# Kernel optimization log

Hardware: AMD Instinct MI355X
Metric: run time of the kernel (lower is better)

Reference implementation:

```python
import jax, jax.numpy as jnp
import numpy as np
import math

IN_F, OUT_F = 512, 512
N_HEADS, N_SPLITS = 32, 4
N = 1024
DELTA_SCALE = 0.1


def setup_inputs() -> dict:
    key = jax.random.key(0)
    k_x, k_h, k_s, k_w = jax.random.split(key, 4)
    stdv = 1.0 / math.sqrt(OUT_F)
    inputs = {
        "input": jax.random.normal(k_x, (N, IN_F), dtype=jnp.float32),
        "head_ix": jax.random.randint(k_h, (N,), 0, N_HEADS, dtype=jnp.int32),
        "split_ix": jax.random.randint(k_s, (N,), 0, N_SPLITS, dtype=jnp.int32),
        # learned parameters (EmbeddingTensor tables)
        "weight": jax.random.uniform(k_w, (N_HEADS, IN_F, OUT_F), dtype=jnp.float32,
                                     minval=-stdv, maxval=stdv),
        "delta_weight": jnp.zeros((N_HEADS * N_SPLITS, IN_F, OUT_F), dtype=jnp.float32),
        "bias": jnp.zeros((N_HEADS, OUT_F), dtype=jnp.float32),
    }
    return inputs


def reference(input, head_ix, split_ix, weight, delta_weight, bias):
    # per-sample weight: base[head] + 0.1 * delta[head * n_splits + split]
    w = weight[head_ix] + delta_weight[head_ix * N_SPLITS + split_ix] * DELTA_SCALE  # [N, in, out]
    # batched vector-matrix multiply + per-head bias
    return jnp.einsum('ab,abc->ac', input, w) + bias[head_ix]  # [N, out]
```

## Files before the change

kernel.cpp:

```cpp
#include <hip/hip_runtime.h>

#define N_SAMP   1024
#define IN_F     512
#define OUT_F    512
#define N_HEADS  32
#define N_SPLITS 4
#define N_GROUPS (N_HEADS * N_SPLITS)
#define DELTA_SCALE 0.1f

__global__ __launch_bounds__(256, 4) void lms_fused(
    const float* __restrict__ X, const int* __restrict__ head_ix,
    const int* __restrict__ split_ix, const float* __restrict__ W,
    const float* __restrict__ D, const float* __restrict__ bias,
    float* __restrict__ out)
{
    constexpr int J    = 16;
    constexpr int KQ   = 8;
    constexpr int KT   = IN_F / KQ;
    constexpr int NST  = KT / 4;
    constexpr int NOUT = (J * 32) / 256;

    __shared__ float buf[J * IN_F];
    __shared__ int   list[N_SAMP];
    __shared__ int   wsum[4];

    const int g    = blockIdx.y;
    const int h    = g / N_SPLITS;
    const int c0   = blockIdx.x * 64;
    const int tid  = threadIdx.x;
    const int c2   = tid & 31;
    const int kq   = tid >> 5;
    const int lane = tid & 63;
    const int wave = tid >> 6;

    int run = 0;
    for (int r = 0; r < N_SAMP / 256; ++r) {
        const int i   = r * 256 + tid;
        const int key = head_ix[i] * N_SPLITS + split_ix[i];
        const bool hit = (key == g);
        const unsigned long long m = __ballot(hit);
        if (lane == 0) wsum[wave] = __popcll(m);
        __syncthreads();
        int base = run;
        for (int w = 0; w < 4; ++w)
            if (w < wave) base += wsum[w];
        if (hit)
            list[base + __popcll(m & ((1ULL << lane) - 1ULL))] = i;
        run += wsum[0] + wsum[1] + wsum[2] + wsum[3];
        __syncthreads();
    }
    const int total = run;
    if (total == 0) return;

    const size_t roff = (size_t)(kq * KT) * OUT_F + c0 + c2 * 2;
    const float* wp = W + (size_t)h * (IN_F * OUT_F) + roff;
    const float* dp = D + (size_t)g * (IN_F * OUT_F) + roff;

    for (int s0 = 0; s0 < total; s0 += J) {
        const int nc = min(total - s0, J);

        __syncthreads();
        for (int i = tid; i < J * (IN_F / 4); i += 256) {
            const int s = i >> 7, q = i & 127;
            float4 v = make_float4(0.f, 0.f, 0.f, 0.f);
            if (s < nc)
                v = *(const float4*)(X + (size_t)list[s0 + s] * IN_F + q * 4);
            *(float4*)(&buf[s * IN_F + q * 4]) = v;
        }
        __syncthreads();

        float2 acc[J];
#pragma unroll
        for (int j = 0; j < J; ++j) { acc[j].x = 0.f; acc[j].y = 0.f; }

        float2 wb[2][4], db[2][4];
#pragma unroll
        for (int u = 0; u < 4; ++u) {
            wb[0][u] = *(const float2*)(wp + (size_t)u * OUT_F);
            db[0][u] = *(const float2*)(dp + (size_t)u * OUT_F);
        }

#pragma unroll 2
        for (int st = 0; st < NST; ++st) {
            const int nx = (st + 1 < NST) ? st + 1 : NST - 1;
            const int nb = (st + 1) & 1, cb = st & 1;
            const float* wn = wp + (size_t)(nx * 4) * OUT_F;
            const float* dn = dp + (size_t)(nx * 4) * OUT_F;
#pragma unroll
            for (int u = 0; u < 4; ++u) {
                wb[nb][u] = *(const float2*)(wn + (size_t)u * OUT_F);
                db[nb][u] = *(const float2*)(dn + (size_t)u * OUT_F);
            }

            float2 rc[4];
#pragma unroll
            for (int u = 0; u < 4; ++u) {
                rc[u].x = wb[cb][u].x + DELTA_SCALE * db[cb][u].x;
                rc[u].y = wb[cb][u].y + DELTA_SCALE * db[cb][u].y;
            }

            const float* xb = &buf[kq * KT + st * 4];
#pragma unroll
            for (int j = 0; j < J; ++j) {
                const float4 xv = *(const float4*)(xb + j * IN_F);
                acc[j].x += xv.x * rc[0].x; acc[j].y += xv.x * rc[0].y;
                acc[j].x += xv.y * rc[1].x; acc[j].y += xv.y * rc[1].y;
                acc[j].x += xv.z * rc[2].x; acc[j].y += xv.z * rc[2].y;
                acc[j].x += xv.w * rc[3].x; acc[j].y += xv.w * rc[3].y;
            }
        }

        __syncthreads();
        float2* Red = (float2*)buf;
#pragma unroll
        for (int j = 0; j < J; ++j)
            Red[(kq * J + j) * 32 + c2] = acc[j];
        __syncthreads();

#pragma unroll
        for (int t = 0; t < NOUT; ++t) {
            const int oi = t * 256 + tid;
            const int j = oi >> 5, cc = oi & 31;
            if (j < nc) {
                float2 s = make_float2(0.f, 0.f);
#pragma unroll
                for (int q = 0; q < KQ; ++q) {
                    const float2 r = Red[(q * J + j) * 32 + cc];
                    s.x += r.x; s.y += r.y;
                }
                const float2 bv =
                    *(const float2*)(bias + (size_t)h * OUT_F + c0 + cc * 2);
                float* op = out + (size_t)list[s0 + j] * OUT_F + c0 + cc * 2;
                float2 res;
                res.x = s.x + bv.x;
                res.y = s.y + bv.y;
                *(float2*)op = res;
            }
        }
    }
}

extern "C" void kernel_launch(void* const* d_in, const int* in_sizes, int n_in,
                              void* d_out, int out_size, void* d_ws, size_t ws_size,
                              hipStream_t stream) {
    const float* X        = (const float*)d_in[0];
    const int*   head_ix  = (const int*)d_in[1];
    const int*   split_ix = (const int*)d_in[2];
    const float* W        = (const float*)d_in[3];
    const float* D        = (const float*)d_in[4];
    const float* bias     = (const float*)d_in[5];
    float*       out      = (float*)d_out;

    dim3 gf(OUT_F / 64, N_GROUPS);
    lms_fused<<<gf, 256, 0, stream>>>(X, head_ix, split_ix, W, D, bias, out);
}
```

Baseline: 240.0 us.

## Stream full-width weight rows through shared memory and split samples across block pairs

Each block now covers 256 output columns and walks the whole K dimension itself. Eight combined weight rows (W + 0.1*D) per step are staged in a double-buffered shared tile using coalesced float4 loads. This removes the old per-block K-split and the shared-memory cross-partition reduction. The samples of each group are interleaved across two blocks, so each weight/delta slice is fetched by two blocks rather than once per column chunk. The change trades a block-wide barrier every eight rows and fewer, larger blocks (launch bounds lowered to 2) for wider contiguous reads and no reduction phase.

```diff
diff --git a/kernel.cpp b/kernel.cpp
--- a/kernel.cpp
+++ b/kernel.cpp
@@ -8,28 +8,31 @@
 #define N_GROUPS (N_HEADS * N_SPLITS)
 #define DELTA_SCALE 0.1f
 
-__global__ __launch_bounds__(256, 4) void lms_fused(
+__global__ __launch_bounds__(256, 2) void lms_rowstream(
     const float* __restrict__ X, const int* __restrict__ head_ix,
     const int* __restrict__ split_ix, const float* __restrict__ W,
     const float* __restrict__ D, const float* __restrict__ bias,
     float* __restrict__ out)
 {
-    constexpr int J    = 16;
-    constexpr int KQ   = 8;
-    constexpr int KT   = IN_F / KQ;
-    constexpr int NST  = KT / 4;
-    constexpr int NOUT = (J * 32) / 256;
+    constexpr int J    = 8;
+    constexpr int NSG  = 2;
+    constexpr int HC   = 256;
+    constexpr int RPS  = 8;
+    constexpr int NST  = IN_F / RPS;
 
-    __shared__ float buf[J * IN_F];
+    __shared__ float Xs[J][IN_F];
+    __shared__ float rcb[2][RPS][HC];
     __shared__ int   list[N_SAMP];
     __shared__ int   wsum[4];
 
     const int g    = blockIdx.y;
-    const int h    = g / N_SPLITS;
-    const int c0   = blockIdx.x * 64;
+    const int h    = g >> 2;
+    const int sg   = blockIdx.x & 1;
+    const int ch   = blockIdx.x >> 1;
+    const int c0   = ch * HC;
     const int tid  = threadIdx.x;
-    const int c2   = tid & 31;
-    const int kq   = tid >> 5;
+    const int c2   = tid & 127;
+    const int jh   = tid >> 7;
     const int lane = tid & 63;
     const int wave = tid >> 6;
 
@@ -50,90 +53,102 @@
         __syncthreads();
     }
     const int total = run;
-    if (total == 0) return;
+    const int cnt = (total > sg) ? ((total - 1 - sg) / NSG + 1) : 0;
+    if (cnt == 0) return;
 
-    const size_t roff = (size_t)(kq * KT) * OUT_F + c0 + c2 * 2;
-    const float* wp = W + (size_t)h * (IN_F * OUT_F) + roff;
-    const float* dp = D + (size_t)g * (IN_F * OUT_F) + roff;
+    const float* wbase = W + (size_t)h * (IN_F * OUT_F) + c0;
+    const float* dbase = D + (size_t)g * (IN_F * OUT_F) + c0;
+    const float2 bv = *(const float2*)(bias + (size_t)h * OUT_F + c0 + 2 * c2);
 
-    for (int s0 = 0; s0 < total; s0 += J) {
-        const int nc = min(total - s0, J);
+    for (int cb = 0; cb < cnt; cb += J) {
+        const int nc = min(cnt - cb, J);
 
         __syncthreads();
-        for (int i = tid; i < J * (IN_F / 4); i += 256) {
-            const int s = i >> 7, q = i & 127;
+        for (int f = 0; f < 4; ++f) {
+            const int fid = f * 256 + tid;
+            const int s = fid >> 7, q = fid & 127;
             float4 v = make_float4(0.f, 0.f, 0.f, 0.f);
             if (s < nc)
-                v = *(const float4*)(X + (size_t)list[s0 + s] * IN_F + q * 4);
-            *(float4*)(&buf[s * IN_F + q * 4]) = v;
+                v = *(const float4*)(X + (size_t)list[sg + NSG * (cb + s)] * IN_F + q * 4);
+            *(float4*)(&Xs[s][q * 4]) = v;
         }
-        __syncthreads();
 
-        float2 acc[J];
+        float2 acc[4];
 #pragma unroll
-        for (int j = 0; j < J; ++j) { acc[j].x = 0.f; acc[j].y = 0.f; }
+        for (int jj = 0; jj < 4; ++jj) { acc[jj].x = 0.f; acc[jj].y = 0.f; }
 
-        float2 wb[2][4], db[2][4];
-#pragma unroll
-        for (int u = 0; u < 4; ++u) {
-            wb[0][u] = *(const float2*)(wp + (size_t)u * OUT_F);
-            db[0][u] = *(const float2*)(dp + (size_t)u * OUT_F);
+        const int r0 = tid >> 6,        cc0 = (tid & 63) << 2;
+        const int r1 = (256 + tid) >> 6, cc1 = cc0;
+        float4 wrg[2][2], drg[2][2];
+
+        {
+            const float* wp = wbase;
+            const float* dp = dbase;
+            wrg[0][0] = *(const float4*)(wp + (size_t)r0 * OUT_F + cc0);
+            wrg[0][1] = *(const float4*)(wp + (size_t)r1 * OUT_F + cc1);
+            drg[0][0] = *(const float4*)(dp + (size_t)r0 * OUT_F + cc0);
+            drg[0][1] = *(const float4*)(dp + (size_t)r1 * OUT_F + cc1);
         }
 
 #pragma unroll 2
-        for (int st = 0; st < NST; ++st) {
-            const int nx = (st + 1 < NST) ? st + 1 : NST - 1;
-            const int nb = (st + 1) & 1, cb = st & 1;
-            const float* wn = wp + (size_t)(nx * 4) * OUT_F;
-            const float* dn = dp + (size_t)(nx * 4) * OUT_F;
-#pragma unroll
-            for (int u = 0; u < 4; ++u) {
-                wb[nb][u] = *(const float2*)(wn + (size_t)u * OUT_F);
-                db[nb][u] = *(const float2*)(dn + (size_t)u * OUT_F);
+        for (int t = 0; t < NST; ++t) {
+            const int cur = t & 1, nxt = cur ^ 1;
+            const int k0 = t * RPS;
+
+            if (t + 1 < NST) {
+                const float* wp = wbase + (size_t)(k0 + RPS) * OUT_F;
+                const float* dp = dbase + (size_t)(k0 + RPS) * OUT_F;
+                wrg[nxt][0] = *(const float4*)(wp + (size_t)r0 * OUT_F + cc0);
+                wrg[nxt][1] = *(const float4*)(wp + (size_t)r1 * OUT_F + cc1);
+                drg[nxt][0] = *(const float4*)(dp + (size_t)r0 * OUT_F + cc0);
+                drg[nxt][1] = *(const float4*)(dp + (size_t)r1 * OUT_F + cc1);
             }
 
-            float2 rc[4];
-#pragma unroll
-            for (int u = 0; u < 4; ++u) {
-                rc[u].x = wb[cb][u].x + DELTA_SCALE * db[cb][u].x;
-                rc[u].y = wb[cb][u].y + DELTA_SCALE * db[cb][u].y;
+            {
+                float4 a = wrg[cur][0], b = drg[cur][0];
+                float4 rc0 = make_float4(a.x + DELTA_SCALE * b.x,
+                                         a.y + DELTA_SCALE * b.y,
+                                         a.z + DELTA_SCALE * b.z,
+                                         a.w + DELTA_SCALE * b.w);
+                *(float4*)(&rcb[cur][r0][cc0]) = rc0;
+                a = wrg[cur][1]; b = drg[cur][1];
+                float4 rc1 = make_float4(a.x + DELTA_SCALE * b.x,
+                                         a.y + DELTA_SCALE * b.y,
+                                         a.z + DELTA_SCALE * b.z,
+                                         a.w + DELTA_SCALE * b.w);
+                *(float4*)(&rcb[cur][r1][cc1]) = rc1;
             }
 
-            const float* xb = &buf[kq * KT + st * 4];
+            __syncthreads();
+
+            float2 rr[RPS];
 #pragma unroll
-            for (int j = 0; j < J; ++j) {
-                const float4 xv = *(const float4*)(xb + j * IN_F);
-                acc[j].x += xv.x * rc[0].x; acc[j].y += xv.x * rc[0].y;
-                acc[j].x += xv.y * rc[1].x; acc[j].y += xv.y * rc[1].y;
-                acc[j].x += xv.z * rc[2].x; acc[j].y += xv.z * rc[2].y;
-                acc[j].x += xv.w * rc[3].x; acc[j].y += xv.w * rc[3].y;
+            for (int r = 0; r < RPS; ++r)
+                rr[r] = *(const float2*)(&rcb[cur][r][2 * c2]);
+#pragma unroll
+            for (int jj = 0; jj < 4; ++jj) {
+                const int j = jh * 4 + jj;
+                const float4 xa = *(const float4*)(&Xs[j][k0]);
+                const float4 xb = *(const float4*)(&Xs[j][k0 + 4]);
+                acc[jj].x += xa.x * rr[0].x; acc[jj].y += xa.x * rr[0].y;
+                acc[jj].x += xa.y * rr[1].x; acc[jj].y += xa.y * rr[1].y;
+                acc[jj].x += xa.z * rr[2].x; acc[jj].y += xa.z * rr[2].y;
+                acc[jj].x += xa.w * rr[3].x; acc[jj].y += xa.w * rr[3].y;
+                acc[jj].x += xb.x * rr[4].x; acc[jj].y += xb.x * rr[4].y;
+                acc[jj].x += xb.y * rr[5].x; acc[jj].y += xb.y * rr[5].y;
+                acc[jj].x += xb.z * rr[6].x; acc[jj].y += xb.z * rr[6].y;
+                acc[jj].x += xb.w * rr[7].x; acc[jj].y += xb.w * rr[7].y;
             }
         }
 
-        __syncthreads();
-        float2* Red = (float2*)buf;
 #pragma unroll
-        for (int j = 0; j < J; ++j)
-            Red[(kq * J + j) * 32 + c2] = acc[j];
-        __syncthreads();
-
-#pragma unroll
-        for (int t = 0; t < NOUT; ++t) {
-            const int oi = t * 256 + tid;
-            const int j = oi >> 5, cc = oi & 31;
-            if (j < nc) {
-                float2 s = make_float2(0.f, 0.f);
-#pragma unroll
-                for (int q = 0; q < KQ; ++q) {
-                    const float2 r = Red[(q * J + j) * 32 + cc];
-                    s.x += r.x; s.y += r.y;
-                }
-                const float2 bv =
-                    *(const float2*)(bias + (size_t)h * OUT_F + c0 + cc * 2);
-                float* op = out + (size_t)list[s0 + j] * OUT_F + c0 + cc * 2;
+        for (int jj = 0; jj < 4; ++jj) {
+            const int i = cb + jh * 4 + jj;
+            if (i < cnt) {
+                float* op = out + (size_t)list[sg + NSG * i] * OUT_F + c0 + 2 * c2;
                 float2 res;
-                res.x = s.x + bv.x;
-                res.y = s.y + bv.y;
+                res.x = acc[jj].x + bv.x;
+                res.y = acc[jj].y + bv.y;
                 *(float2*)op = res;
             }
         }
@@ -151,6 +166,6 @@
     const float* bias     = (const float*)d_in[5];
     float*       out      = (float*)d_out;
 
-    dim3 gf(OUT_F / 64, N_GROUPS);
-    lms_fused<<<gf, 256, 0, stream>>>(X, head_ix, split_ix, W, D, bias, out);
+    dim3 gf(4, N_GROUPS);
+    lms_rowstream<<<gf, 256, 0, stream>>>(X, head_ix, split_ix, W, D, bias, out);
 }
```

Result: slower. 263.4 us (+9.7%).

## Split K across blocks with workspace partials and a separate reduce kernel

Applied to the files above, without the earlier changes.

Adds a split-K path. Each block handles one group and one 64-row K slice across all 512 output columns, writes partial sums to a workspace, and a second kernel sums the eight partials and adds bias. This removes the in-block shared-memory reduction and shrinks the X staging per block. It also remaps block indices so neighbouring blocks cover different groups. The cost is an extra kernel launch and about 16 MB of workspace writes and reads. The old fused kernel is kept as a fallback when the workspace is too small.

```diff
diff --git a/kernel.cpp b/kernel.cpp
--- a/kernel.cpp
+++ b/kernel.cpp
@@ -7,6 +7,138 @@
 #define N_SPLITS 4
 #define N_GROUPS (N_HEADS * N_SPLITS)
 #define DELTA_SCALE 0.1f
+
+#define KSPLIT   8
+#define KROWS    (IN_F / KSPLIT)
+#define JC       16
+
+
+__global__ __launch_bounds__(256, 4) void lms_partial(
+    const float* __restrict__ X, const int* __restrict__ head_ix,
+    const int* __restrict__ split_ix, const float* __restrict__ W,
+    const float* __restrict__ D, float* __restrict__ ws)
+{
+    __shared__ float Xs[JC][KROWS];
+    __shared__ int   list[N_SAMP];
+    __shared__ int   wsum[4];
+
+    const int b       = blockIdx.x;
+    const int logical = (b & 7) * 128 + (b >> 3);
+    const int g       = logical >> 3;
+    const int kb      = logical & 7;
+    const int h       = g >> 2;
+
+    const int tid  = threadIdx.x;
+    const int lane = tid & 63;
+    const int wave = tid >> 6;
+
+    int run = 0;
+    for (int r = 0; r < N_SAMP / 256; ++r) {
+        const int i   = r * 256 + tid;
+        const int key = head_ix[i] * N_SPLITS + split_ix[i];
+        const bool hit = (key == g);
+        const unsigned long long m = __ballot(hit);
+        if (lane == 0) wsum[wave] = __popcll(m);
+        __syncthreads();
+        int base = run;
+        for (int w = 0; w < 4; ++w)
+            if (w < wave) base += wsum[w];
+        if (hit)
+            list[base + __popcll(m & ((1ULL << lane) - 1ULL))] = i;
+        run += wsum[0] + wsum[1] + wsum[2] + wsum[3];
+        __syncthreads();
+    }
+    const int total = run;
+    if (total == 0) return;
+
+    const float* wq = W + (size_t)h * (IN_F * OUT_F)
+                    + (size_t)(kb * KROWS) * OUT_F + 2 * tid;
+    const float* dq = D + (size_t)g * (IN_F * OUT_F)
+                    + (size_t)(kb * KROWS) * OUT_F + 2 * tid;
+
+    for (int cb = 0; cb < total; cb += JC) {
+        const int nc = min(total - cb, JC);
+
+        __syncthreads();
+        {
+            const int s  = tid >> 4;
+            const int qq = tid & 15;
+            float4 v = make_float4(0.f, 0.f, 0.f, 0.f);
+            if (s < nc)
+                v = *(const float4*)(X + (size_t)list[cb + s] * IN_F
+                                     + kb * KROWS + qq * 4);
+            *(float4*)(&Xs[s][qq * 4]) = v;
+        }
+        __syncthreads();
+
+        float2 acc[JC];
+#pragma unroll
+        for (int j = 0; j < JC; ++j) { acc[j].x = 0.f; acc[j].y = 0.f; }
+
+        float2 wr[2][4], dr[2][4];
+#pragma unroll
+        for (int f = 0; f < 4; ++f) {
+            wr[0][f] = *(const float2*)(wq + (size_t)f * OUT_F);
+            dr[0][f] = *(const float2*)(dq + (size_t)f * OUT_F);
+        }
+
+        constexpr int NB = KROWS / 4;
+#pragma unroll 2
+        for (int bt = 0; bt < NB; ++bt) {
+            const int cur = bt & 1, nxt = cur ^ 1;
+            const int nr = (bt + 1 < NB) ? (bt + 1) * 4 : bt * 4;
+#pragma unroll
+            for (int f = 0; f < 4; ++f) {
+                wr[nxt][f] = *(const float2*)(wq + (size_t)(nr + f) * OUT_F);
+                dr[nxt][f] = *(const float2*)(dq + (size_t)(nr + f) * OUT_F);
+            }
+
+            float2 rc[4];
+#pragma unroll
+            for (int f = 0; f < 4; ++f) {
+                rc[f].x = wr[cur][f].x + DELTA_SCALE * dr[cur][f].x;
+                rc[f].y = wr[cur][f].y + DELTA_SCALE * dr[cur][f].y;
+            }
+
+#pragma unroll
+            for (int j = 0; j < JC; ++j) {
+                const float4 xv = *(const float4*)(&Xs[j][bt * 4]);
+                acc[j].x += xv.x * rc[0].x; acc[j].y += xv.x * rc[0].y;
+                acc[j].x += xv.y * rc[1].x; acc[j].y += xv.y * rc[1].y;
+                acc[j].x += xv.z * rc[2].x; acc[j].y += xv.z * rc[2].y;
+                acc[j].x += xv.w * rc[3].x; acc[j].y += xv.w * rc[3].y;
+            }
+        }
+
+#pragma unroll
+        for (int j = 0; j < JC; ++j) {
+            if (j < nc) {
+                float* op = ws + ((size_t)kb * N_SAMP + list[cb + j]) * OUT_F
+                          + 2 * tid;
+                *(float2*)op = acc[j];
+            }
+        }
+    }
+}
+
+__global__ __launch_bounds__(256, 4) void lms_reduce(
+    const float* __restrict__ ws, const int* __restrict__ head_ix,
+    const float* __restrict__ bias, float* __restrict__ out)
+{
+    const int gid = blockIdx.x * 256 + threadIdx.x;
+    const int i   = gid >> 7;
+    const int c4  = gid & 127;
+    const int h   = head_ix[i];
+
+    float4 s = *(const float4*)(bias + (size_t)h * OUT_F + 4 * c4);
+#pragma unroll
+    for (int kb = 0; kb < KSPLIT; ++kb) {
+        const float4 p = *(const float4*)(ws + ((size_t)kb * N_SAMP + i) * OUT_F
+                                          + 4 * c4);
+        s.x += p.x; s.y += p.y; s.z += p.z; s.w += p.w;
+    }
+    *(float4*)(out + (size_t)i * OUT_F + 4 * c4) = s;
+}
 
 __global__ __launch_bounds__(256, 4) void lms_fused(
     const float* __restrict__ X, const int* __restrict__ head_ix,
@@ -25,7 +157,7 @@
     __shared__ int   wsum[4];
 
     const int g    = blockIdx.y;
-    const int h    = g / N_SPLITS;
+    const int h    = g >> 2;
     const int c0   = blockIdx.x * 64;
     const int tid  = threadIdx.x;
     const int c2   = tid & 31;
@@ -58,7 +190,6 @@
 
     for (int s0 = 0; s0 < total; s0 += J) {
         const int nc = min(total - s0, J);
-
         __syncthreads();
         for (int i = tid; i < J * (IN_F / 4); i += 256) {
             const int s = i >> 7, q = i & 127;
@@ -91,14 +222,12 @@
                 wb[nb][u] = *(const float2*)(wn + (size_t)u * OUT_F);
                 db[nb][u] = *(const float2*)(dn + (size_t)u * OUT_F);
             }
-
             float2 rc[4];
 #pragma unroll
             for (int u = 0; u < 4; ++u) {
                 rc[u].x = wb[cb][u].x + DELTA_SCALE * db[cb][u].x;
                 rc[u].y = wb[cb][u].y + DELTA_SCALE * db[cb][u].y;
             }
-
             const float* xb = &buf[kq * KT + st * 4];
 #pragma unroll
             for (int j = 0; j < J; ++j) {
@@ -151,6 +280,15 @@
     const float* bias     = (const float*)d_in[5];
     float*       out      = (float*)d_out;
 
-    dim3 gf(OUT_F / 64, N_GROUPS);
-    lms_fused<<<gf, 256, 0, stream>>>(X, head_ix, split_ix, W, D, bias, out);
-}
+    const size_t ws_need = (size_t)KSPLIT * N_SAMP * OUT_F * sizeof(float);
+    if (ws_size >= ws_need) {
+        float* ws = (float*)d_ws;
+        lms_partial<<<dim3(N_GROUPS * KSPLIT), 256, 0, stream>>>(
+            X, head_ix, split_ix, W, D, ws);
+        lms_reduce<<<dim3((N_SAMP * OUT_F / 4) / 256), 256, 0, stream>>>(
+            ws, head_ix, bias, out);
+    } else {
+        dim3 gf(OUT_F / 64, N_GROUPS);
+        lms_fused<<<gf, 256, 0, stream>>>(X, head_ix, split_ix, W, D, bias, out);
+    }
+}
```

After: 269.2 us. 12.2% more time.

## Widen per-thread column tile to float4, split K across 16 groups, nontemporal loads

Applied to the files above, without the earlier changes.

Each thread now covers four output columns with 16-wide vector accumulators, and the K dimension is split into 16 slices instead of 8, with 12 samples per chunk instead of 16. The delta-weight loads and the output stores use nontemporal hints. The cross-slice reduction becomes a two-stage shared-memory add, and the combined weight for the next step is computed after the FMAs to hide load latency. The aim is wider global loads and more parallelism per group, in exchange for lower occupancy (launch bounds 2) and more passes over the weights when a group has more than 12 samples, since each chunk rereads the whole weight slice.

```diff
diff --git a/kernel.cpp b/kernel.cpp
--- a/kernel.cpp
+++ b/kernel.cpp
@@ -8,28 +8,37 @@
 #define N_GROUPS (N_HEADS * N_SPLITS)
 #define DELTA_SCALE 0.1f
 
-__global__ __launch_bounds__(256, 4) void lms_fused(
+
+typedef float f32x4 __attribute__((ext_vector_type(4)));
+
+__device__ __forceinline__ f32x4 nt_load4(const float* p) {
+    return __builtin_nontemporal_load((const f32x4*)p);
+}
+__device__ __forceinline__ void nt_store4(float* p, f32x4 v) {
+    __builtin_nontemporal_store(v, (f32x4*)p);
+}
+
+__global__ __launch_bounds__(256, 2) void lms_fused_nt_w4(
     const float* __restrict__ X, const int* __restrict__ head_ix,
     const int* __restrict__ split_ix, const float* __restrict__ W,
     const float* __restrict__ D, const float* __restrict__ bias,
     float* __restrict__ out)
 {
-    constexpr int J    = 16;
-    constexpr int KQ   = 8;
+    constexpr int J    = 12;
+    constexpr int KQ   = 16;
     constexpr int KT   = IN_F / KQ;
     constexpr int NST  = KT / 4;
-    constexpr int NOUT = (J * 32) / 256;
 
     __shared__ float buf[J * IN_F];
     __shared__ int   list[N_SAMP];
     __shared__ int   wsum[4];
 
     const int g    = blockIdx.y;
-    const int h    = g / N_SPLITS;
+    const int h    = g >> 2;
     const int c0   = blockIdx.x * 64;
     const int tid  = threadIdx.x;
-    const int c2   = tid & 31;
-    const int kq   = tid >> 5;
+    const int c4   = tid & 15;
+    const int kq   = tid >> 4;
     const int lane = tid & 63;
     const int wave = tid >> 6;
 
@@ -52,7 +61,7 @@
     const int total = run;
     if (total == 0) return;
 
-    const size_t roff = (size_t)(kq * KT) * OUT_F + c0 + c2 * 2;
+    const size_t roff = (size_t)(kq * KT) * OUT_F + c0 + c4 * 4;
     const float* wp = W + (size_t)h * (IN_F * OUT_F) + roff;
     const float* dp = D + (size_t)g * (IN_F * OUT_F) + roff;
 
@@ -60,7 +69,9 @@
         const int nc = min(total - s0, J);
 
         __syncthreads();
-        for (int i = tid; i < J * (IN_F / 4); i += 256) {
+#pragma unroll
+        for (int f = 0; f < 6; ++f) {
+            const int i = f * 256 + tid;
             const int s = i >> 7, q = i & 127;
             float4 v = make_float4(0.f, 0.f, 0.f, 0.f);
             if (s < nc)
@@ -69,72 +80,79 @@
         }
         __syncthreads();
 
-        float2 acc[J];
+        f32x4 acc[J];
 #pragma unroll
-        for (int j = 0; j < J; ++j) { acc[j].x = 0.f; acc[j].y = 0.f; }
+        for (int j = 0; j < J; ++j) acc[j] = (f32x4)0.f;
 
-        float2 wb[2][4], db[2][4];
+        f32x4 rc[2][4];
+        {
+            f32x4 w0[4], d0[4];
 #pragma unroll
-        for (int u = 0; u < 4; ++u) {
-            wb[0][u] = *(const float2*)(wp + (size_t)u * OUT_F);
-            db[0][u] = *(const float2*)(dp + (size_t)u * OUT_F);
+            for (int u = 0; u < 4; ++u) {
+                w0[u] = *(const f32x4*)(wp + (size_t)u * OUT_F);
+                d0[u] = nt_load4(dp + (size_t)u * OUT_F);
+            }
+#pragma unroll
+            for (int u = 0; u < 4; ++u)
+                rc[0][u] = w0[u] + DELTA_SCALE * d0[u];
         }
 
-#pragma unroll 2
+#pragma unroll
         for (int st = 0; st < NST; ++st) {
-            const int nx = (st + 1 < NST) ? st + 1 : NST - 1;
-            const int nb = (st + 1) & 1, cb = st & 1;
-            const float* wn = wp + (size_t)(nx * 4) * OUT_F;
-            const float* dn = dp + (size_t)(nx * 4) * OUT_F;
+            const int cb = st & 1, nb = cb ^ 1;
+            const int nr = (st + 1 < NST) ? (st + 1) * 4 : st * 4;
+            f32x4 wl[4], dl[4];
 #pragma unroll
             for (int u = 0; u < 4; ++u) {
-                wb[nb][u] = *(const float2*)(wn + (size_t)u * OUT_F);
-                db[nb][u] = *(const float2*)(dn + (size_t)u * OUT_F);
-            }
-
-            float2 rc[4];
-#pragma unroll
-            for (int u = 0; u < 4; ++u) {
-                rc[u].x = wb[cb][u].x + DELTA_SCALE * db[cb][u].x;
-                rc[u].y = wb[cb][u].y + DELTA_SCALE * db[cb][u].y;
+                wl[u] = *(const f32x4*)(wp + (size_t)(nr + u) * OUT_F);
+                dl[u] = nt_load4(dp + (size_t)(nr + u) * OUT_F);
             }
 
             const float* xb = &buf[kq * KT + st * 4];
 #pragma unroll
             for (int j = 0; j < J; ++j) {
                 const float4 xv = *(const float4*)(xb + j * IN_F);
-                acc[j].x += xv.x * rc[0].x; acc[j].y += xv.x * rc[0].y;
-                acc[j].x += xv.y * rc[1].x; acc[j].y += xv.y * rc[1].y;
-                acc[j].x += xv.z * rc[2].x; acc[j].y += xv.z * rc[2].y;
-                acc[j].x += xv.w * rc[3].x; acc[j].y += xv.w * rc[3].y;
+                acc[j] += xv.x * rc[cb][0];
+                acc[j] += xv.y * rc[cb][1];
+                acc[j] += xv.z * rc[cb][2];
+                acc[j] += xv.w * rc[cb][3];
             }
+
+#pragma unroll
+            for (int u = 0; u < 4; ++u)
+                rc[nb][u] = wl[u] + DELTA_SCALE * dl[u];
         }
 
         __syncthreads();
-        float2* Red = (float2*)buf;
+        f32x4* Red = (f32x4*)buf;
+        if (kq < 8) {
 #pragma unroll
-        for (int j = 0; j < J; ++j)
-            Red[(kq * J + j) * 32 + c2] = acc[j];
+            for (int j = 0; j < J; ++j)
+                Red[(kq * J + j) * 16 + c4] = acc[j];
+        }
+        __syncthreads();
+        if (kq >= 8) {
+            const int q = kq - 8;
+#pragma unroll
+            for (int j = 0; j < J; ++j) {
+                f32x4 r = Red[(q * J + j) * 16 + c4];
+                Red[(q * J + j) * 16 + c4] = r + acc[j];
+            }
+        }
         __syncthreads();
 
+        if (tid < J * 16) {
+            const int j  = tid >> 4;
+            const int cc = tid & 15;
+            if (j < nc) {
+                f32x4 s = (f32x4)0.f;
 #pragma unroll
-        for (int t = 0; t < NOUT; ++t) {
-            const int oi = t * 256 + tid;
-            const int j = oi >> 5, cc = oi & 31;
-            if (j < nc) {
-                float2 s = make_float2(0.f, 0.f);
-#pragma unroll
-                for (int q = 0; q < KQ; ++q) {
-                    const float2 r = Red[(q * J + j) * 32 + cc];
-                    s.x += r.x; s.y += r.y;
-                }
-                const float2 bv =
-                    *(const float2*)(bias + (size_t)h * OUT_F + c0 + cc * 2);
-                float* op = out + (size_t)list[s0 + j] * OUT_F + c0 + cc * 2;
-                float2 res;
-                res.x = s.x + bv.x;
-                res.y = s.y + bv.y;
-                *(float2*)op = res;
+                for (int q = 0; q < 8; ++q)
+                    s += Red[(q * J + j) * 16 + cc];
+                const f32x4 bv = *(const f32x4*)(bias + (size_t)h * OUT_F
+                                                 + c0 + cc * 4);
+                float* op = out + (size_t)list[s0 + j] * OUT_F + c0 + cc * 4;
+                nt_store4(op, s + bv);
             }
         }
     }
@@ -152,5 +170,5 @@
     float*       out      = (float*)d_out;
 
     dim3 gf(OUT_F / 64, N_GROUPS);
-    lms_fused<<<gf, 256, 0, stream>>>(X, head_ix, split_ix, W, D, bias, out);
+    lms_fused_nt_w4<<<gf, 256, 0, stream>>>(X, head_ix, split_ix, W, D, bias, out);
 }
```

Measured after the change: 229.7 us. 1.04x faster.
